# Kernel tuning notes

Measured on AMD Instinct MI355X. Metric: run time of the kernel, lower is better.

## Reference

```python
import jax, jax.numpy as jnp
import numpy as np

B, P, D, O = 262144, 512, 40, 256  # batch, n_prototypes, latent_size (pinned to 40), output_size


def setup_inputs() -> dict:
    key = jax.random.key(0)
    k1, k2, k3, k4 = jax.random.split(key, 4)
    inp = jax.random.normal(k1, (B, D), dtype=jnp.float32)
    # nn.init.uniform_ default is U[0,1)
    prototypes = jax.random.uniform(k2, (P, D), dtype=jnp.float32)
    # nn.Linear default init: U[-1/sqrt(in), 1/sqrt(in)]
    lim = 1.0 / np.sqrt(P)
    W = jax.random.uniform(k3, (O, P), dtype=jnp.float32, minval=-lim, maxval=lim)
    b = jax.random.uniform(k4, (O,), dtype=jnp.float32, minval=-lim, maxval=lim)
    return {"input": inp, "prototypes": prototypes, "W": W, "b": b}


def reference(input, prototypes, W, b):
    # Faithful to original: x[i] = sqrt( sum over ALL prototypes and dims of (input_i - prototypes)**2 )
    # i.e. a per-row SCALAR broadcast across the prototype axis (original code sums over all axes).
    x = input.astype(jnp.float32).reshape(input.shape[0], 40)
    n_proto = prototypes.shape[0]
    row_sq = jnp.sum(x * x, axis=1)                 # [B]
    proto_sum = jnp.sum(prototypes, axis=0)         # [D]
    proto_sq = jnp.sum(prototypes * prototypes)     # scalar
    d2 = n_proto * row_sq - 2.0 * (x @ proto_sum) + proto_sq  # [B]
    dist = jnp.sqrt(d2)                             # [B]
    xmat = jnp.broadcast_to(dist[:, None], (x.shape[0], n_proto))  # [B, P]
    out = xmat @ W.T + b                            # [B, O]
    return (xmat, out)
```

## Files before the change

### kernel.cpp

```cpp
#include <hip/hip_runtime.h>


#define B_ROWS 262144
#define P_N 512
#define D_N 40
#define O_N 256


__global__ __launch_bounds__(256) void pre_kernel(const float* __restrict__ proto,
                                                  const float* __restrict__ W,
                                                  float* __restrict__ ws) {
    __shared__ float sm[4];
    const int t = threadIdx.x;
    const int blk = blockIdx.x;
    const int lane = t & 63, w = t >> 6;
    if (blk < D_N) {
        float s = 0.f, sq = 0.f;
        for (int p = t; p < P_N; p += 256) {
            float v = proto[p * D_N + blk];
            s += v;
            sq += v * v;
        }
        #pragma unroll
        for (int off = 32; off; off >>= 1) {
            s += __shfl_xor(s, off);
            sq += __shfl_xor(sq, off);
        }
        if (lane == 0) sm[w] = s;
        __syncthreads();
        if (t == 0) ws[blk] = sm[0] + sm[1] + sm[2] + sm[3];
        __syncthreads();
        if (lane == 0) sm[w] = sq;
        __syncthreads();
        if (t == 0) ws[296 + blk] = sm[0] + sm[1] + sm[2] + sm[3];
    } else {
        const int o = blk - D_N;
        float s = 0.f;
        for (int p = t; p < P_N; p += 256) s += W[(long)o * P_N + p];
        #pragma unroll
        for (int off = 32; off; off >>= 1) s += __shfl_xor(s, off);
        if (lane == 0) sm[w] = s;
        __syncthreads();
        if (t == 0) ws[40 + o] = sm[0] + sm[1] + sm[2] + sm[3];
    }
}

__global__ __launch_bounds__(256) void main_kernel(const float* __restrict__ x,
                                                   const float* __restrict__ b,
                                                   const float* __restrict__ ws,
                                                   float* __restrict__ xmat,
                                                   float* __restrict__ outp) {
    __shared__ float sdist[256];
    const int t = threadIdx.x;
    const long base = (long)blockIdx.x * 256;

    const float4* __restrict__ xr  = reinterpret_cast<const float4*>(x + (base + t) * D_N);
    const float4* __restrict__ ps4 = reinterpret_cast<const float4*>(ws);
    const float4* __restrict__ pq4 = reinterpret_cast<const float4*>(ws + 296);
    float sumsq = 0.f, dot = 0.f, psq = 0.f;
    #pragma unroll
    for (int k = 0; k < D_N / 4; ++k) {
        const float4 v = xr[k];
        const float4 p = ps4[k];
        const float4 q = pq4[k];
        sumsq = fmaf(v.x, v.x, fmaf(v.y, v.y, fmaf(v.z, v.z, fmaf(v.w, v.w, sumsq))));
        dot   = fmaf(v.x, p.x, fmaf(v.y, p.y, fmaf(v.z, p.z, fmaf(v.w, p.w, dot))));
        psq  += q.x + q.y + q.z + q.w;
    }
    sdist[t] = sqrtf(fmaf(512.f, sumsq, fmaf(-2.f, dot, psq)));
    __syncthreads();

    float4* __restrict__ xm = reinterpret_cast<float4*>(xmat + base * P_N);
    #pragma unroll 8
    for (int i = 0; i < 128; ++i) {
        const int j = i * 256 + t;
        const float d = sdist[j >> 7];
        xm[j] = make_float4(d, d, d, d);
    }

    const float4 wv = reinterpret_cast<const float4*>(ws + 40)[t & 63];
    const float4 bv = reinterpret_cast<const float4*>(b)[t & 63];
    float4* __restrict__ om = reinterpret_cast<float4*>(outp + base * O_N);
    #pragma unroll 8
    for (int i = 0; i < 64; ++i) {
        const int j = i * 256 + t;
        const float d = sdist[j >> 6];
        om[j] = make_float4(fmaf(d, wv.x, bv.x), fmaf(d, wv.y, bv.y),
                            fmaf(d, wv.z, bv.z), fmaf(d, wv.w, bv.w));
    }
}

extern "C" void kernel_launch(void* const* d_in, const int* in_sizes, int n_in,
                              void* d_out, int out_size, void* d_ws, size_t ws_size,
                              hipStream_t stream) {
    const float* inp   = (const float*)d_in[0];
    const float* proto = (const float*)d_in[1];
    const float* W     = (const float*)d_in[2];
    const float* b     = (const float*)d_in[3];
    float* ws   = (float*)d_ws;
    float* xmat = (float*)d_out;
    float* outp = xmat + (long)B_ROWS * P_N;

    hipLaunchKernelGGL(pre_kernel, dim3(296), dim3(256), 0, stream, proto, W, ws);
    hipLaunchKernelGGL(main_kernel, dim3(B_ROWS / 256), dim3(256), 0, stream,
                       inp, b, ws, xmat, outp);
}
```

Measured before the change: 164.8 us.

## Split distance computation into separate kernel before pure store-streaming kernel

```diff
diff --git a/kernel.cpp b/kernel.cpp
--- a/kernel.cpp
+++ b/kernel.cpp
@@ -45,15 +45,67 @@
     }
 }
 
-__global__ __launch_bounds__(256) void main_kernel(const float* __restrict__ x,
-                                                   const float* __restrict__ b,
+__global__ __launch_bounds__(256) void dist_kernel(const float* __restrict__ x,
                                                    const float* __restrict__ ws,
-                                                   float* __restrict__ xmat,
-                                                   float* __restrict__ outp) {
+                                                   float* __restrict__ dist) {
+    const long i = (long)blockIdx.x * 256 + threadIdx.x;
+    const float4* __restrict__ xr  = reinterpret_cast<const float4*>(x + i * D_N);
+    const float4* __restrict__ ps4 = reinterpret_cast<const float4*>(ws);
+    const float4* __restrict__ pq4 = reinterpret_cast<const float4*>(ws + 296);
+    float sumsq = 0.f, dot = 0.f, psq = 0.f;
+    #pragma unroll
+    for (int k = 0; k < D_N / 4; ++k) {
+        const float4 v = xr[k];
+        const float4 p = ps4[k];
+        const float4 q = pq4[k];
+        sumsq = fmaf(v.x, v.x, fmaf(v.y, v.y, fmaf(v.z, v.z, fmaf(v.w, v.w, sumsq))));
+        dot   = fmaf(v.x, p.x, fmaf(v.y, p.y, fmaf(v.z, p.z, fmaf(v.w, p.w, dot))));
+        psq  += q.x + q.y + q.z + q.w;
+    }
+    dist[i] = sqrtf(fmaf(512.f, sumsq, fmaf(-2.f, dot, psq)));
+}
+
+__global__ __launch_bounds__(256) void stream_kernel(const float* __restrict__ b,
+                                                     const float* __restrict__ ws,
+                                                     const float* __restrict__ dist,
+                                                     float* __restrict__ xmat,
+                                                     float* __restrict__ outp) {
+    __shared__ float sd[128];
+    const int t = threadIdx.x;
+    const long rbase = (long)blockIdx.x * 128;
+    if (t < 32)
+        reinterpret_cast<float4*>(sd)[t] =
+            reinterpret_cast<const float4*>(dist + rbase)[t];
+    const float4 wv = reinterpret_cast<const float4*>(ws + 40)[t & 63];
+    const float4 bv = reinterpret_cast<const float4*>(b)[t & 63];
+    __syncthreads();
+
+    float4* __restrict__ xm = reinterpret_cast<float4*>(xmat + rbase * P_N);
+    #pragma unroll 8
+    for (int i = 0; i < 64; ++i) {
+        const int j = i * 256 + t;
+        const float d = sd[j >> 7];
+        xm[j] = make_float4(d, d, d, d);
+    }
+
+    float4* __restrict__ om = reinterpret_cast<float4*>(outp + rbase * O_N);
+    #pragma unroll 8
+    for (int i = 0; i < 32; ++i) {
+        const int j = i * 256 + t;
+        const float d = sd[j >> 6];
+        om[j] = make_float4(fmaf(d, wv.x, bv.x), fmaf(d, wv.y, bv.y),
+                            fmaf(d, wv.z, bv.z), fmaf(d, wv.w, bv.w));
+    }
+}
+
+__global__ __launch_bounds__(256) void fused_kernel(const float* __restrict__ x,
+                                                    const float* __restrict__ b,
+                                                    const float* __restrict__ ws,
+                                                    float* __restrict__ xmat,
+                                                    float* __restrict__ outp) {
     __shared__ float sdist[256];
     const int t = threadIdx.x;
     const long base = (long)blockIdx.x * 256;
-
     const float4* __restrict__ xr  = reinterpret_cast<const float4*>(x + (base + t) * D_N);
     const float4* __restrict__ ps4 = reinterpret_cast<const float4*>(ws);
     const float4* __restrict__ pq4 = reinterpret_cast<const float4*>(ws + 296);
@@ -77,7 +129,6 @@
         const float d = sdist[j >> 7];
         xm[j] = make_float4(d, d, d, d);
     }
-
     const float4 wv = reinterpret_cast<const float4*>(ws + 40)[t & 63];
     const float4 bv = reinterpret_cast<const float4*>(b)[t & 63];
     float4* __restrict__ om = reinterpret_cast<float4*>(outp + base * O_N);
@@ -102,6 +153,15 @@
     float* outp = xmat + (long)B_ROWS * P_N;
 
     hipLaunchKernelGGL(pre_kernel, dim3(296), dim3(256), 0, stream, proto, W, ws);
-    hipLaunchKernelGGL(main_kernel, dim3(B_ROWS / 256), dim3(256), 0, stream,
-                       inp, b, ws, xmat, outp);
+
+    if (ws_size >= (size_t)(512 + B_ROWS + 64) * sizeof(float)) {
+        float* dist = ws + 512;
+        hipLaunchKernelGGL(dist_kernel, dim3(B_ROWS / 256), dim3(256), 0, stream,
+                           inp, ws, dist);
+        hipLaunchKernelGGL(stream_kernel, dim3(B_ROWS / 128), dim3(256), 0, stream,
+                           b, ws, dist, xmat, outp);
+    } else {
+        hipLaunchKernelGGL(fused_kernel, dim3(B_ROWS / 256), dim3(256), 0, stream,
+                           inp, b, ws, xmat, outp);
+    }
 }
```

New measurement: 162.6 us. Within noise of the previous version (-1.3%).
